# Kernel optimization log

Hardware: AMD Instinct MI355X
Metric: run time of the kernel (lower is better)

## Reference

```python
import jax, jax.numpy as jnp
import numpy as np

B, S, EMB, HID, VOCAB = 64, 4096, 20, 20, 256
TEMPERATURE = 0.001


def setup_inputs():
    key = jax.random.key(0)
    ks = jax.random.split(key, 16)
    rn = lambda k, shape: jax.random.normal(k, shape, jnp.float32) * 0.1
    return {
        'inp': jax.random.randint(ks[0], (B, S, 2), 0, 2**31 - 1, dtype=jnp.int32),
        'h0': jnp.zeros((1, B, HID), jnp.float32),
        'c0': jnp.zeros((1, B, HID), jnp.float32),
        'pc_emb': rn(ks[1], (4, VOCAB, EMB)),
        'addr_emb': rn(ks[2], (4, VOCAB, EMB)),
        'enc_W': rn(ks[3], (EMB, 4 * EMB)),
        'enc_b': rn(ks[4], (EMB,)),
        'W_ih': rn(ks[5], (4 * HID, 2 * EMB)),
        'W_hh': rn(ks[6], (4 * HID, HID)),
        'b_ih': rn(ks[7], (4 * HID,)),
        'b_hh': rn(ks[8], (4 * HID,)),
        'dec_W': rn(ks[9], (4, VOCAB, HID)),
        'dec_b': rn(ks[10], (4, VOCAB)),
        'd1_W': rn(ks[11], (10, 3 * EMB)),
        'd1_b': rn(ks[12], (10,)),
        'd2_W': rn(ks[13], (2, 10)),
        'd2_b': rn(ks[14], (2,)),
    }


def _byte_embed(vals, tables):
    # vals: (B,S) int32; vectorized replacement for get_bytes_2d + 4 gathers
    shifts = jnp.array([24, 16, 8, 0], dtype=jnp.int32)  # big-endian byte order
    byts = (vals[..., None] >> shifts) & 0xFF            # (B,S,4)
    embs = [tables[i][byts[..., i]] for i in range(4)]   # each (B,S,EMB)
    return jnp.concatenate(embs, axis=-1)                # (B,S,4*EMB)


def reference(inp, h0, c0, pc_emb, addr_emb, enc_W, enc_b, W_ih, W_hh,
              b_ih, b_hh, dec_W, dec_b, d1_W, d1_b, d2_W, d2_b):
    encode = lambda x: jax.nn.sigmoid(x @ enc_W.T + enc_b)  # Encoder MLP
    pc_e = encode(_byte_embed(inp[:, :, 0], pc_emb))         # (B,S,EMB)
    ad_e = encode(_byte_embed(inp[:, :, 1], addr_emb))       # (B,S,EMB)
    emb = jnp.concatenate([pc_e, ad_e], axis=-1)             # (B,S,2*EMB)

    # get_distribution_vector: KDE sample mean -> deterministic expectation
    # (= mean of the fitted data); detached in the original (input.detach()).
    dist_vector = jax.lax.stop_gradient(jnp.mean(emb, axis=1))  # (B,2*EMB)

    # LSTM (torch gate order i,f,g,o)
    def step(carry, x_t):
        h, c = carry
        gates = x_t @ W_ih.T + b_ih + h @ W_hh.T + b_hh
        i, f, g, o = jnp.split(gates, 4, axis=-1)
        c = jax.nn.sigmoid(f) * c + jax.nn.sigmoid(i) * jnp.tanh(g)
        h = jax.nn.sigmoid(o) * jnp.tanh(c)
        return (h, c), None

    (h, _), _ = jax.lax.scan(step, (h0[0], c0[0]), jnp.swapaxes(emb, 0, 1))
    hidden = h[None]                                          # (1,B,HID)

    # Decoder_lstm: 4 heads; softmax over dim=1 of (1,B,V) == batch axis
    logits = jnp.einsum('obh,kvh->kobv', hidden, dec_W) + dec_b[:, None, None, :]
    probs = jax.nn.softmax(logits / TEMPERATURE, axis=2)      # (4,1,B,V)

    # get_freq_rec: probs[i] @ address_embeddings[i].weight, concat, encode
    byte_e = jnp.einsum('kobv,kve->obke', probs, addr_emb)    # (1,B,4,EMB)
    fe = encode(byte_e.reshape(1, inp.shape[0], 4 * EMB))[0]  # (B,EMB)
    fr_in = jnp.concatenate([fe, dist_vector], axis=-1)       # (B,3*EMB)
    freq_rec = jax.nn.relu(fr_in @ d1_W.T + d1_b) @ d2_W.T + d2_b  # (B,2)
    return probs, logits, freq_rec[:, 0], freq_rec[:, 1]
```

## Files before the change

### kernel.cpp

```cpp
#include <hip/hip_runtime.h>
#include <math.h>

#define BB 64
#define SS 4096
#define OF_G    0
#define OF_BG   40960
#define OF_DIST 41056
#define OF_HFIN 43616
#define OF_WS   44896
#define OF_X    48096
#define WS_NEEDED_FLOATS (OF_X + (size_t)BB * SS * 80 + 8 * 80)

#define L2E 1.4426950408889634f

typedef float v2f __attribute__((ext_vector_type(2)));

__device__ __forceinline__ float fast_rcp(float x) { return __builtin_amdgcn_rcpf(x); }
__device__ __forceinline__ float fast_exp2(float x) { return __builtin_amdgcn_exp2f(x); }
__device__ __forceinline__ float sigm_prec(float x) { return 1.0f / (1.0f + __expf(-x)); }
#define RL(v, m) __int_as_float(__builtin_amdgcn_readlane(__float_as_int(v), (m)))

__global__ __launch_bounds__(256) void k_init(const float* __restrict__ pc_emb,
    const float* __restrict__ addr_emb, const float* __restrict__ enc_W,
    const float* __restrict__ b_ih, const float* __restrict__ b_hh,
    const float* __restrict__ W_ih, float* __restrict__ ws) {
  int gid = blockIdx.x * 256 + threadIdx.x;
  if (gid < 2048) {
    int t = gid >> 10;
    int i = (gid >> 8) & 3;
    int byt = gid & 255;
    const float* tab = (t == 0 ? pc_emb : addr_emb) + (i * 256 + byt) * 20;
    float tv[20];
#pragma unroll
    for (int m = 0; m < 20; m++) tv[m] = tab[m];
    float* Grow = ws + OF_G + gid * 20;
#pragma unroll
    for (int j = 0; j < 20; j++) {
      float acc = 0.f;
#pragma unroll
      for (int m = 0; m < 20; m++) acc = fmaf(enc_W[j * 80 + i * 20 + m], tv[m], acc);
      Grow[j] = acc;
    }
  } else if (gid < 2048 + 80) {
    int g = gid - 2048;
    float sc = (g >= 40 && g < 60) ? (2.0f * L2E) : (-L2E);
    ws[OF_BG + g] = (b_ih[g] + b_hh[g]) * sc;
  } else if (gid < 2048 + 80 + 2560) {
    ws[OF_DIST + (gid - 2128)] = 0.f;
  } else if (gid < 2048 + 80 + 2560 + 3200) {
    int q = gid - 4688;
    int g = q / 40;
    float sc = (g >= 40 && g < 60) ? (2.0f * L2E) : (-L2E);
    ws[OF_WS + q] = W_ih[q] * sc;
  }
}

__global__ __launch_bounds__(64) void k_embed(const int* __restrict__ inp,
    const float* __restrict__ enc_b, float* __restrict__ ws) {
  __shared__ float lds[80 * 65];
  int b = blockIdx.x >> 6;
  int schunk = (blockIdx.x & 63) << 6;
  int t = threadIdx.x;
  int s = schunk + t;
  unsigned v0 = (unsigned)inp[(b * SS + s) * 2 + 0];
  unsigned v1 = (unsigned)inp[(b * SS + s) * 2 + 1];
  const float4* G4 = (const float4*)(ws + OF_G);
  float e[40];
#pragma unroll
  for (int st = 0; st < 2; st++) {
    unsigned v = (st == 0) ? v0 : v1;
    int by0 = (int)(v >> 24);
    int by1 = (int)((v >> 16) & 255u);
    int by2 = (int)((v >> 8) & 255u);
    int by3 = (int)(v & 255u);
    int r0 = ((st * 4 + 0) * 256 + by0) * 5;
    int r1 = ((st * 4 + 1) * 256 + by1) * 5;
    int r2 = ((st * 4 + 2) * 256 + by2) * 5;
    int r3 = ((st * 4 + 3) * 256 + by3) * 5;
    float4 acc[5];
#pragma unroll
    for (int p = 0; p < 5; p++) {
      float4 a = G4[r0 + p];
      float4 bq = G4[r1 + p];
      float4 cq = G4[r2 + p];
      float4 d = G4[r3 + p];
      acc[p] = make_float4(a.x + bq.x + cq.x + d.x, a.y + bq.y + cq.y + d.y,
                           a.z + bq.z + cq.z + d.z, a.w + bq.w + cq.w + d.w);
    }
    const float* af = (const float*)acc;
#pragma unroll
    for (int j = 0; j < 20; j++)
      e[st * 20 + j] = sigm_prec(enc_b[j] + af[j]);
  }
  const float* Wsc = ws + OF_WS;
  const float* bg = ws + OF_BG;
#pragma unroll 4
  for (int g = 0; g < 80; g++) {
    float a = bg[g];
#pragma unroll
    for (int d = 0; d < 40; d++) a = fmaf(Wsc[g * 40 + d], e[d], a);
    lds[g * 65 + t] = a;
  }
  __syncthreads();
  float4* XF4 = (float4*)(ws + OF_X) + (size_t)(b * SS + schunk) * 20;
#pragma unroll
  for (int it = 0; it < 20; it++) {
    int q = it * 64 + t;
    int tok = q / 20;
    int jf = q - tok * 20;
    float4 vv;
    vv.x = lds[(0  + jf) * 65 + tok];
    vv.y = lds[(20 + jf) * 65 + tok];
    vv.z = lds[(40 + jf) * 65 + tok];
    vv.w = lds[(60 + jf) * 65 + tok];
    XF4[q] = vv;
  }
  __syncthreads();
  float* eT = lds;
#pragma unroll
  for (int d = 0; d < 40; d++) eT[d * 66 + t] = e[d];
  __syncthreads();
  if (t < 40) {
    float ssum = 0.f;
#pragma unroll 8
    for (int tok = 0; tok < 64; tok++) ssum += eT[t * 66 + tok];
    atomicAdd(ws + OF_DIST + b * 40 + t, ssum);
  }
}

__global__ __launch_bounds__(64) void k_lstm(const float* __restrict__ h0,
    const float* __restrict__ c0, const float* __restrict__ W_hh,
    float* __restrict__ ws) {
  int b = blockIdx.x;
  int l = threadIdx.x;
  int j = (l & 31) < 20 ? (l & 31) : 19;
  float q0 = (float)l, q1 = (float)l;
  asm("v_permlane32_swap_b32 %0, %1" : "+v"(q0), "+v"(q1));
  int dir = (__builtin_amdgcn_readfirstlane(__float_as_int(q0)) == 0) ? 0 : 1;
  int sp = ((l >> 5) ^ dir) & 1;
  v2f wAB[20];
#pragma unroll
  for (int m = 0; m < 20; m++) {
    float wa = (sp == 0) ? W_hh[(0 * 20 + j) * 20 + m] * (-L2E)
                         : W_hh[(2 * 20 + j) * 20 + m] * (2.0f * L2E);
    float wb = (sp == 0) ? W_hh[(1 * 20 + j) * 20 + m] * (-L2E)
                         : W_hh[(3 * 20 + j) * 20 + m] * (-L2E);
    wAB[m] = (v2f){wa, wb};
  }
  v2f kA = (sp == 0) ? (v2f){1.0f, 1.0f} : (v2f){-4.0f * L2E, 1.0f};
  v2f kB = (sp == 0) ? (v2f){0.0f, 0.0f} : (v2f){2.0f * L2E, 0.0f};
  float h = h0[b * 20 + j];
  float cs = c0[b * 20 + j] * (2.0f * L2E);
  const float2* Xp = (const float2*)(ws + OF_X) + (size_t)b * SS * 40 + j * 2 + sp;
  float2 xb[8];
#pragma unroll
  for (int p = 0; p < 8; p++) xb[p] = Xp[p * 40];
  const float2* Xq = Xp;
  for (int s = 0; s < SS; s += 8) {
#pragma unroll
    for (int u = 0; u < 8; u++) {
      float2 x2 = xb[u];
      xb[u] = Xq[(u + 8) * 40];
      float hm[20];
#pragma unroll
      for (int m = 0; m < 4; m++) hm[m] = RL(h, m);
      v2f aA = (v2f){x2.x, x2.y};
      v2f aB = (v2f){0.f, 0.f};
#pragma unroll
      for (int m = 0; m < 10; m++) {
        hm[m + 4] = RL(h, m + 4);
        v2f hv = (v2f){hm[m], hm[m]};
        aA = __builtin_elementwise_fma(wAB[m], hv, aA);
      }
#pragma unroll
      for (int m = 10; m < 20; m++) {
        if (m + 4 < 20) hm[m + 4] = RL(h, m + 4);
        v2f hv = (v2f){hm[m], hm[m]};
        aB = __builtin_elementwise_fma(wAB[m], hv, aB);
      }
      v2f a = aA + aB;
      float e0 = fast_exp2(a.x);
      float e1 = fast_exp2(a.y);
      v2f den = (v2f){1.0f + e0, 1.0f + e1};
      v2f r = (v2f){fast_rcp(den.x), fast_rcp(den.y)};
      v2f res = __builtin_elementwise_fma(r, kA, kB);
      float d0 = res.x, s0 = res.x;
      float d1 = res.y, s1 = res.y;
      asm("v_permlane32_swap_b32 %0, %1" : "+v"(d0), "+v"(s0));
      asm("v_permlane32_swap_b32 %0, %1" : "+v"(d1), "+v"(s1));
      cs = fmaf(d1, cs, d0 * s0);
      float tc = fmaf(-2.0f, fast_rcp(1.0f + fast_exp2(cs)), 1.0f);
      h = s1 * tc;
    }
    Xq += 8 * 40;
  }
  if (l < 20) ws[OF_HFIN + b * 20 + l] = h;
}

__global__ __launch_bounds__(256) void k_dec(const float* __restrict__ dec_W,
    const float* __restrict__ dec_b, float* __restrict__ out,
    const float* __restrict__ ws) {
  int wid = blockIdx.x * 4 + (threadIdx.x >> 6);
  int lane = threadIdx.x & 63;
  int k = wid >> 8;
  int v = wid & 255;
  const float* hp = ws + OF_HFIN + lane * 20;
  const float* wp = dec_W + (k * 256 + v) * 20;
  float l = dec_b[k * 256 + v];
#pragma unroll
  for (int jj = 0; jj < 20; jj++) l = fmaf(hp[jj], wp[jj], l);
  float x = l / 0.001f;
  float mx = x;
#pragma unroll
  for (int off = 32; off; off >>= 1) mx = fmaxf(mx, __shfl_xor(mx, off));
  float ex = __expf(x - mx);
  float sm = ex;
#pragma unroll
  for (int off = 32; off; off >>= 1) sm += __shfl_xor(sm, off);
  float p = ex / sm;
  int oidx = (k * 64 + lane) * 256 + v;
  out[oidx] = p;
  out[65536 + oidx] = l;
}

__global__ __launch_bounds__(128) void k_freq(const float* __restrict__ addr_emb,
    const float* __restrict__ enc_W, const float* __restrict__ enc_b,
    const float* __restrict__ d1_W, const float* __restrict__ d1_b,
    const float* __restrict__ d2_W, const float* __restrict__ d2_b,
    float* __restrict__ out, const float* __restrict__ ws) {
  __shared__ float be[80];
  __shared__ float fr[60];
  __shared__ float r1[10];
  int b = blockIdx.x;
  int t = threadIdx.x;
  if (t < 80) {
    int k = t / 20, e2 = t % 20;
    const float* pp = out + (k * 64 + b) * 256;
    const float* ap = addr_emb + (k * 256) * 20 + e2;
    float acc = 0.f;
#pragma unroll 8
    for (int v = 0; v < 256; v++) acc = fmaf(pp[v], ap[v * 20], acc);
    be[t] = acc;
  }
  __syncthreads();
  if (t < 20) {
    float acc = enc_b[t];
#pragma unroll
    for (int d = 0; d < 80; d++) acc = fmaf(enc_W[t * 80 + d], be[d], acc);
    fr[t] = 1.0f / (1.0f + __expf(-acc));
  } else if (t < 60) {
    fr[t] = ws[OF_DIST + b * 40 + (t - 20)] * (1.0f / 4096.0f);
  }
  __syncthreads();
  if (t < 10) {
    float acc = d1_b[t];
#pragma unroll
    for (int d = 0; d < 60; d++) acc = fmaf(d1_W[t * 60 + d], fr[d], acc);
    r1[t] = acc > 0.f ? acc : 0.f;
  }
  __syncthreads();
  if (t < 2) {
    float acc = d2_b[t];
#pragma unroll
    for (int r = 0; r < 10; r++) acc = fmaf(d2_W[t * 10 + r], r1[r], acc);
    out[131072 + t * 64 + b] = acc;
  }
}

extern "C" void kernel_launch(void* const* d_in, const int* in_sizes, int n_in,
                              void* d_out, int out_size, void* d_ws, size_t ws_size,
                              hipStream_t stream) {
  const int*   inp    = (const int*)  d_in[0];
  const float* h0     = (const float*)d_in[1];
  const float* c0     = (const float*)d_in[2];
  const float* pc_emb = (const float*)d_in[3];
  const float* addr_e = (const float*)d_in[4];
  const float* enc_W  = (const float*)d_in[5];
  const float* enc_b  = (const float*)d_in[6];
  const float* W_ih   = (const float*)d_in[7];
  const float* W_hh   = (const float*)d_in[8];
  const float* b_ih   = (const float*)d_in[9];
  const float* b_hh   = (const float*)d_in[10];
  const float* dec_W  = (const float*)d_in[11];
  const float* dec_b  = (const float*)d_in[12];
  const float* d1_W   = (const float*)d_in[13];
  const float* d1_b   = (const float*)d_in[14];
  const float* d2_W   = (const float*)d_in[15];
  const float* d2_b   = (const float*)d_in[16];
  float* out = (float*)d_out;
  float* ws  = (float*)d_ws;

  if (ws_size < WS_NEEDED_FLOATS * sizeof(float)) return;

  hipLaunchKernelGGL(k_init, dim3(31), dim3(256), 0, stream,
                     pc_emb, addr_e, enc_W, b_ih, b_hh, W_ih, ws);
  hipLaunchKernelGGL(k_embed, dim3(4096), dim3(64), 0, stream, inp, enc_b, ws);
  hipLaunchKernelGGL(k_lstm, dim3(64), dim3(64), 0, stream, h0, c0, W_hh, ws);
  hipLaunchKernelGGL(k_dec, dim3(256), dim3(256), 0, stream, dec_W, dec_b, out, ws);
  hipLaunchKernelGGL(k_freq, dim3(64), dim3(128), 0, stream,
                     addr_e, enc_W, enc_b, d1_W, d1_b, d2_W, d2_b, out, ws);
}
```

Before: 867.0 us.

## Pack two timesteps per float4 in LSTM input layout and streamline readlane chain

The precomputed input-projection buffer is rearranged so that each lane's gate inputs for two consecutive timesteps sit in one float4. The LSTM kernel then issues half as many loads, each twice as wide, and runs two steps per load. The step body moves into a macro that fetches the hidden-state broadcasts one readlane ahead instead of prefetching four. This is meant to cut load-instruction overhead and register pressure on the serial recurrence. The prefetch depth now covers twice as many steps per buffered entry, and the workspace tail padding is enlarged to match.

After: 846.8 us. -2.3%, faster.

```diff
diff --git a/kernel.cpp b/kernel.cpp
--- a/kernel.cpp
+++ b/kernel.cpp
@@ -9,7 +9,7 @@
 #define OF_HFIN 43616
 #define OF_WS   44896
 #define OF_X    48096
-#define WS_NEEDED_FLOATS (OF_X + (size_t)BB * SS * 80 + 8 * 80)
+#define WS_NEEDED_FLOATS (OF_X + (size_t)BB * SS * 80 + 16 * 80)
 
 #define L2E 1.4426950408889634f
 
@@ -102,17 +102,22 @@
     lds[g * 65 + t] = a;
   }
   __syncthreads();
-  float4* XF4 = (float4*)(ws + OF_X) + (size_t)(b * SS + schunk) * 20;
+  float4* XF4 = (float4*)(ws + OF_X) + ((size_t)b * 2048 + (schunk >> 1)) * 40;
 #pragma unroll
   for (int it = 0; it < 20; it++) {
     int q = it * 64 + t;
-    int tok = q / 20;
-    int jf = q - tok * 20;
+    int lp = q / 40;
+    int lanepos = q - lp * 40;
+    int j = lanepos >> 1;
+    int sp = lanepos & 1;
+    int g0 = sp * 40 + j;
+    int g1 = g0 + 20;
+    int tok0 = lp * 2, tok1 = tok0 + 1;
     float4 vv;
-    vv.x = lds[(0  + jf) * 65 + tok];
-    vv.y = lds[(20 + jf) * 65 + tok];
-    vv.z = lds[(40 + jf) * 65 + tok];
-    vv.w = lds[(60 + jf) * 65 + tok];
+    vv.x = lds[g0 * 65 + tok0];
+    vv.y = lds[g1 * 65 + tok0];
+    vv.z = lds[g0 * 65 + tok1];
+    vv.w = lds[g1 * 65 + tok1];
     XF4[q] = vv;
   }
   __syncthreads();
@@ -127,6 +132,38 @@
     atomicAdd(ws + OF_DIST + b * 40 + t, ssum);
   }
 }
+
+#define LSTM_STEP(xA, xB) do {                                                 \
+    float hc = RL(h, 0);                                                       \
+    v2f aA = (v2f){(xA), (xB)};                                                \
+    v2f aB = (v2f){0.f, 0.f};                                                  \
+    _Pragma("unroll")                                                          \
+    for (int m = 0; m < 10; m++) {                                             \
+      float hn = RL(h, m + 1);                                                 \
+      v2f hv = (v2f){hc, hc};                                                  \
+      aA = __builtin_elementwise_fma(wAB[m], hv, aA);                          \
+      hc = hn;                                                                 \
+    }                                                                          \
+    _Pragma("unroll")                                                          \
+    for (int m = 10; m < 20; m++) {                                            \
+      float hn = (m < 19) ? RL(h, m + 1) : 0.f;                                \
+      v2f hv = (v2f){hc, hc};                                                  \
+      aB = __builtin_elementwise_fma(wAB[m], hv, aB);                          \
+      hc = hn;                                                                 \
+    }                                                                          \
+    v2f a = aA + aB;                                                           \
+    float e0 = fast_exp2(a.x);                                                 \
+    float e1 = fast_exp2(a.y);                                                 \
+    v2f r = (v2f){fast_rcp(1.0f + e0), fast_rcp(1.0f + e1)};                   \
+    v2f res = __builtin_elementwise_fma(r, kA, kB);                            \
+    float d0 = res.x, s0 = res.x;                                              \
+    float d1 = res.y, s1 = res.y;                                              \
+    asm("v_permlane32_swap_b32 %0, %1" : "+v"(d0), "+v"(s0));                  \
+    asm("v_permlane32_swap_b32 %0, %1" : "+v"(d1), "+v"(s1));                  \
+    cs = fmaf(d1, cs, d0 * s0);                                                \
+    float tc = fmaf(-2.0f, fast_rcp(1.0f + fast_exp2(cs)), 1.0f);              \
+    h = s1 * tc;                                                               \
+  } while (0)
 
 __global__ __launch_bounds__(64) void k_lstm(const float* __restrict__ h0,
     const float* __restrict__ c0, const float* __restrict__ W_hh,
@@ -151,46 +188,18 @@
   v2f kB = (sp == 0) ? (v2f){0.0f, 0.0f} : (v2f){2.0f * L2E, 0.0f};
   float h = h0[b * 20 + j];
   float cs = c0[b * 20 + j] * (2.0f * L2E);
-  const float2* Xp = (const float2*)(ws + OF_X) + (size_t)b * SS * 40 + j * 2 + sp;
-  float2 xb[8];
+  const float4* Xp = (const float4*)(ws + OF_X) + (size_t)b * 2048 * 40 + (j * 2 + sp);
+  float4 xb[8];
 #pragma unroll
   for (int p = 0; p < 8; p++) xb[p] = Xp[p * 40];
-  const float2* Xq = Xp;
-  for (int s = 0; s < SS; s += 8) {
+  const float4* Xq = Xp;
+  for (int pr = 0; pr < 2048; pr += 8) {
 #pragma unroll
     for (int u = 0; u < 8; u++) {
-      float2 x2 = xb[u];
+      float4 x4 = xb[u];
       xb[u] = Xq[(u + 8) * 40];
-      float hm[20];
-#pragma unroll
-      for (int m = 0; m < 4; m++) hm[m] = RL(h, m);
-      v2f aA = (v2f){x2.x, x2.y};
-      v2f aB = (v2f){0.f, 0.f};
-#pragma unroll
-      for (int m = 0; m < 10; m++) {
-        hm[m + 4] = RL(h, m + 4);
-        v2f hv = (v2f){hm[m], hm[m]};
-        aA = __builtin_elementwise_fma(wAB[m], hv, aA);
-      }
-#pragma unroll
-      for (int m = 10; m < 20; m++) {
-        if (m + 4 < 20) hm[m + 4] = RL(h, m + 4);
-        v2f hv = (v2f){hm[m], hm[m]};
-        aB = __builtin_elementwise_fma(wAB[m], hv, aB);
-      }
-      v2f a = aA + aB;
-      float e0 = fast_exp2(a.x);
-      float e1 = fast_exp2(a.y);
-      v2f den = (v2f){1.0f + e0, 1.0f + e1};
-      v2f r = (v2f){fast_rcp(den.x), fast_rcp(den.y)};
-      v2f res = __builtin_elementwise_fma(r, kA, kB);
-      float d0 = res.x, s0 = res.x;
-      float d1 = res.y, s1 = res.y;
-      asm("v_permlane32_swap_b32 %0, %1" : "+v"(d0), "+v"(s0));
-      asm("v_permlane32_swap_b32 %0, %1" : "+v"(d1), "+v"(s1));
-      cs = fmaf(d1, cs, d0 * s0);
-      float tc = fmaf(-2.0f, fast_rcp(1.0f + fast_exp2(cs)), 1.0f);
-      h = s1 * tc;
+      LSTM_STEP(x4.x, x4.y);
+      LSTM_STEP(x4.z, x4.w);
     }
     Xq += 8 * 40;
   }
```
